# Kernel optimization log

Measured on AMD Instinct MI355X. Metric: run time of the kernel, lower is better.

Reference implementation:

```python
import jax, jax.numpy as jnp
import numpy as np

N, E, H, C, G = 10000, 20000, 12, 768, 64  # nodes, edges, heads, per-head dim, graphs
NEG_SLOPE = 0.2


def _gat_layer(x, W, a_src, a_dst, b, src, dst):
    # x: [N, 768], W: [768, H*C], a_src/a_dst: [H, C], b: [C]
    h = (x @ W).reshape(-1, H, C)                      # [N, H, C]
    s = jnp.einsum('nhc,hc->nh', h, a_src)             # alpha_src per node
    d = jnp.einsum('nhc,hc->nh', h, a_dst)             # alpha_dst per node
    e = jax.nn.leaky_relu(s[src] + d[dst], NEG_SLOPE)  # [Etot, H]
    # segment softmax over incoming edges of each destination node
    m = jax.lax.stop_gradient(jax.ops.segment_max(e, dst, num_segments=N))
    ex = jnp.exp(e - m[dst])
    den = jax.ops.segment_sum(ex, dst, num_segments=N)
    alpha = ex / (den[dst] + 1e-16)                    # [Etot, H]
    out = jax.ops.segment_sum(h[src] * alpha[:, :, None], dst, num_segments=N)
    return out.mean(axis=1) + b                        # concat=False -> head mean, [N, C]


def setup_inputs() -> dict:
    key = jax.random.key(0)
    ks = jax.random.split(key, 16)
    sc = 0.02
    f32 = jnp.float32
    return {
        'x': jax.random.normal(ks[0], (N, 768), f32),
        'edge_index': jax.random.randint(ks[1], (2, E), 0, N),
        'batch': jnp.sort(jax.random.randint(ks[2], (N,), 0, G)),
        'W1': (jax.random.normal(ks[3], (768, H * C), f32) * sc),
        'a_src1': (jax.random.normal(ks[4], (H, C), f32) * sc),
        'a_dst1': (jax.random.normal(ks[5], (H, C), f32) * sc),
        'b1': jnp.zeros((C,), f32),
        'W2': (jax.random.normal(ks[6], (768, H * C), f32) * sc),
        'a_src2': (jax.random.normal(ks[7], (H, C), f32) * sc),
        'a_dst2': (jax.random.normal(ks[8], (H, C), f32) * sc),
        'b2': jnp.zeros((C,), f32),
        'mlp_w1': (jax.random.normal(ks[9], (768, 128), f32) * sc),
        'mlp_b1': jnp.zeros((128,), f32),
        'mlp_w2': (jax.random.normal(ks[10], (128, 4), f32) * sc),
        'mlp_b2': jnp.zeros((4,), f32),
    }


def reference(x, edge_index, batch, W1, a_src1, a_dst1, b1, W2, a_src2, a_dst2, b2,
              mlp_w1, mlp_b1, mlp_w2, mlp_b2):
    loops = jnp.arange(N)                               # GATConv add_self_loops=True
    src = jnp.concatenate([edge_index[0], loops])
    dst = jnp.concatenate([edge_index[1], loops])
    h = _gat_layer(x, W1, a_src1, a_dst1, b1, src, dst)
    h = _gat_layer(h, W2, a_src2, a_dst2, b2, src, dst)
    # scatter_mean over graph assignment
    ssum = jax.ops.segment_sum(h, batch, num_segments=G)
    cnt = jax.ops.segment_sum(jnp.ones((N,), h.dtype), batch, num_segments=G)
    g = ssum / jnp.maximum(cnt, 1.0)[:, None]           # [G, 768]
    z = jax.nn.relu(g @ mlp_w1 + mlp_b1)
    return z @ mlp_w2 + mlp_b2                          # [G, 4] logits
```

## Files before the change

kernel.cpp:

```cpp
#include <hip/hip_runtime.h>
#include <stdint.h>

typedef unsigned short u16;
typedef unsigned int   u32;

#define NNODES 10000
#define NEDGES 20000
#define ETOT   30000
#define NHEADS 12
#define CDIM   768
#define FDIM   768
#define KDIM   9216
#define NGRAPH 64
#define MPAD   10112
#define NEG_SLOPE 0.2f
#define DMAX   32

typedef __attribute__((ext_vector_type(8))) short short8;
typedef __attribute__((ext_vector_type(4))) float f32x4;

__device__ __forceinline__ u16 f32_bf16(float f) {
  u32 u = __float_as_uint(f);
  u = (u + 0x7FFFu + ((u >> 16) & 1u)) >> 16;
  return (u16)u;
}
__device__ __forceinline__ float bf16_f32(u16 v) {
  return __uint_as_float(((u32)v) << 16);
}

__global__ void k_count(const int* __restrict__ dste, int* __restrict__ counts) {
  int e = blockIdx.x * blockDim.x + threadIdx.x;
  if (e >= ETOT) return;
  int dst;
  if (e < NEDGES) dst = dste[e]; else dst = e - NEDGES;
  atomicAdd(&counts[dst], 1);
}

__global__ void k_scan(const int* __restrict__ counts, int* __restrict__ offs) {
  __shared__ int part[256];
  int t = threadIdx.x;
  const int chunk = 40;
  int beg = t * chunk;
  int end = beg + chunk; if (end > NNODES) end = NNODES;
  int s = 0;
  for (int i = beg; i < end && i < NNODES; i++) s += counts[i];
  part[t] = s;
  __syncthreads();
  for (int d = 1; d < 256; d <<= 1) {
    int v = (t >= d) ? part[t - d] : 0;
    __syncthreads();
    part[t] += v;
    __syncthreads();
  }
  int base = (t == 0) ? 0 : part[t - 1];
  for (int i = beg; i < end && i < NNODES; i++) { offs[i] = base; base += counts[i]; }
  if (t == 255) offs[NNODES] = base;
}

__global__ void k_seed(const int* __restrict__ offs, int* __restrict__ cursor) {
  int n = blockIdx.x * blockDim.x + threadIdx.x;
  if (n < NNODES) cursor[n] = offs[n];
}

__global__ void k_scatter(const int* __restrict__ dste, int* __restrict__ cursor,
                          int* __restrict__ elist) {
  int e = blockIdx.x * blockDim.x + threadIdx.x;
  if (e >= ETOT) return;
  int dst;
  if (e < NEDGES) dst = dste[e]; else dst = e - NEDGES;
  int pos = atomicAdd(&cursor[dst], 1);
  elist[pos] = e;
}

__global__ void k_U(const float* __restrict__ W, const float* __restrict__ a_src,
                    const float* __restrict__ a_dst, float* __restrict__ Ut) {
  int k = blockIdx.x;
  int t = threadIdx.x, w = t >> 6, l = t & 63;
  const float* Wrow = W + (size_t)k * KDIM;
#pragma unroll
  for (int q = 0; q < 6; q++) {
    int o = w * 6 + q;
    int h = (o < 12) ? o : o - 12;
    const float* av = (o < 12) ? (a_src + h * CDIM) : (a_dst + h * CDIM);
    const float* wr = Wrow + h * CDIM;
    float p = 0.f;
    for (int c = l; c < CDIM; c += 64) p += wr[c] * av[c];
#pragma unroll
    for (int d = 32; d > 0; d >>= 1) p += __shfl_down(p, d, 64);
    if (l == 0) Ut[o * FDIM + k] = p;
  }
}

__global__ void k_sd(const float* __restrict__ xin, const float* __restrict__ Ut,
                     float* __restrict__ sd, u16* __restrict__ xbf) {
  __shared__ float UtS[24 * FDIM];
  int t = threadIdx.x, w = t >> 6, l = t & 63;
  const float4* U4 = (const float4*)Ut;
  float4* S4 = (float4*)UtS;
  for (int i = t; i < 24 * FDIM / 4; i += 256) S4[i] = U4[i];
  __syncthreads();
#pragma unroll
  for (int rep = 0; rep < 5; rep++) {
    int n = blockIdx.x * 20 + w * 5 + rep;
    if (n >= NNODES) continue;
    const float* xr = xin + (size_t)n * FDIM;
    float4 x0 = *(const float4*)(xr + 4 * l);
    float4 x1 = *(const float4*)(xr + 4 * l + 256);
    float4 x2 = *(const float4*)(xr + 4 * l + 512);
    u16* xb = xbf + (size_t)n * FDIM + 4 * l;
    ushort4 p0, p1, p2;
    p0.x = f32_bf16(x0.x); p0.y = f32_bf16(x0.y); p0.z = f32_bf16(x0.z); p0.w = f32_bf16(x0.w);
    p1.x = f32_bf16(x1.x); p1.y = f32_bf16(x1.y); p1.z = f32_bf16(x1.z); p1.w = f32_bf16(x1.w);
    p2.x = f32_bf16(x2.x); p2.y = f32_bf16(x2.y); p2.z = f32_bf16(x2.z); p2.w = f32_bf16(x2.w);
    *(ushort4*)xb = p0;
    *(ushort4*)(xb + 256) = p1;
    *(ushort4*)(xb + 512) = p2;
#pragma unroll
    for (int o = 0; o < 24; o++) {
      const float4* up = (const float4*)(UtS + o * FDIM + 4 * l);
      float4 u0 = up[0];
      float4 u1 = up[64];
      float4 u2 = up[128];
      float a = x0.x * u0.x + x0.y * u0.y + x0.z * u0.z + x0.w * u0.w
              + x1.x * u1.x + x1.y * u1.y + x1.z * u1.z + x1.w * u1.w
              + x2.x * u2.x + x2.y * u2.y + x2.z * u2.z + x2.w * u2.w;
#pragma unroll
      for (int d = 32; d > 0; d >>= 1) a += __shfl_xor(a, d, 64);
      if (l == 0) sd[n * 24 + o] = a;
    }
  }
}

__global__ void k_trans(const float* __restrict__ W, u16* __restrict__ Bt) {
  int kt = blockIdx.x * 32, jt = blockIdx.y * 32;
  int tx = threadIdx.x, ty = threadIdx.y;
  __shared__ float tile[32][33];
#pragma unroll
  for (int r = 0; r < 4; r++)
    tile[ty + 8 * r][tx] = W[(size_t)(kt + ty + 8 * r) * KDIM + jt + tx];
  __syncthreads();
#pragma unroll
  for (int r = 0; r < 4; r++)
    Bt[(size_t)(jt + ty + 8 * r) * FDIM + kt + tx] = f32_bf16(tile[tx][ty + 8 * r]);
}

__global__ __launch_bounds__(256, 2) void k_gemm(const u16* __restrict__ A,
    const u16* __restrict__ B, u16* __restrict__ C) {
  __shared__ __align__(16) u16 As[2][128 * 32];
  __shared__ __align__(16) u16 Bs[2][256 * 32];
  int t = threadIdx.x;
  int w = t >> 6, l = t & 63;
  int col0 = blockIdx.x * 256;
  int row0 = blockIdx.y * 128;
  int wm = (w >> 1) * 64;
  int wn = (w & 1) * 128;
  f32x4 acc[4][8] = {};
  int idx0 = t * 8;
  int idx1 = idx0 + 2048;
  const u16* Ag0 = A + (size_t)(row0 + (idx0 >> 5)) * FDIM + (idx0 & 31);
  const u16* Ag1 = A + (size_t)(row0 + (idx1 >> 5)) * FDIM + (idx1 & 31);
  const u16* Bg0 = B + (size_t)(col0 + (idx0 >> 5)) * FDIM + (idx0 & 31);
  const u16* Bg1 = B + (size_t)(col0 + ((idx0 + 2048) >> 5)) * FDIM + (idx0 & 31);
  const u16* Bg2 = B + (size_t)(col0 + ((idx0 + 4096) >> 5)) * FDIM + (idx0 & 31);
  const u16* Bg3 = B + (size_t)(col0 + ((idx0 + 6144) >> 5)) * FDIM + (idx0 & 31);
  int lr = l & 15, lk = (l >> 4) * 8;

  short8 ra0, ra1, rb0, rb1, rb2, rb3;
  auto gload = [&](int k0) {
    ra0 = *(const short8*)(Ag0 + k0);
    ra1 = *(const short8*)(Ag1 + k0);
    rb0 = *(const short8*)(Bg0 + k0);
    rb1 = *(const short8*)(Bg1 + k0);
    rb2 = *(const short8*)(Bg2 + k0);
    rb3 = *(const short8*)(Bg3 + k0);
  };
  auto swrite = [&](int buf) {
    *(short8*)(&As[buf][idx0]) = ra0;
    *(short8*)(&As[buf][idx1]) = ra1;
    *(short8*)(&Bs[buf][idx0]) = rb0;
    *(short8*)(&Bs[buf][idx0 + 2048]) = rb1;
    *(short8*)(&Bs[buf][idx0 + 4096]) = rb2;
    *(short8*)(&Bs[buf][idx0 + 6144]) = rb3;
  };

  gload(0);
  swrite(0);
  gload(32);
  __syncthreads();
  const int NIT = FDIM / 32;
  int cur = 0;
  for (int it = 0; it < NIT; it++) {
    short8 af[4], bf[8];
#pragma unroll
    for (int i = 0; i < 4; i++) af[i] = *(const short8*)(&As[cur][(wm + i * 16 + lr) * 32 + lk]);
#pragma unroll
    for (int j = 0; j < 8; j++) bf[j] = *(const short8*)(&Bs[cur][(wn + j * 16 + lr) * 32 + lk]);
#pragma unroll
    for (int i = 0; i < 4; i++)
#pragma unroll
      for (int j = 0; j < 8; j++)
        acc[i][j] = __builtin_amdgcn_mfma_f32_16x16x32_bf16(af[i], bf[j], acc[i][j], 0, 0, 0);
    if (it + 1 < NIT) {
      swrite(cur ^ 1);
      if (it + 2 < NIT) gload((it + 2) * 32);
    }
    __syncthreads();
    cur ^= 1;
  }

  int lg = l >> 4;
#pragma unroll
  for (int i = 0; i < 4; i++)
#pragma unroll
    for (int j = 0; j < 8; j++) {
      int col = col0 + wn + j * 16 + lr;
#pragma unroll
      for (int r = 0; r < 4; r++) {
        int row = row0 + wm + i * 16 + lg * 4 + r;
        C[(size_t)row * KDIM + col] = f32_bf16(acc[i][j][r]);
      }
    }
}

__global__ void k_att(const u16* __restrict__ Hbig, const int* __restrict__ ei,
                      const int* __restrict__ offs, const int* __restrict__ elist,
                      const float* __restrict__ sd, const float* __restrict__ bias,
                      float* __restrict__ out) {
  int t = threadIdx.x, w = t >> 6, l = t & 63;
  int n = blockIdx.x * 4 + w;
  __shared__ int   srcsS[4][DMAX];
  __shared__ float alphS[4][NHEADS * DMAX];
  if (n >= NNODES) return;
  int* srcs = srcsS[w];
  float* alph = alphS[w];
  int beg = offs[n];
  int deg = offs[n + 1] - beg;
  if (deg > DMAX) deg = DMAX;
  if (l < deg) {
    int e = elist[beg + l];
    srcs[l] = (e < NEDGES) ? ei[e] : e - NEDGES;
  }
  __builtin_amdgcn_wave_barrier();
  for (int p = l; p < deg * NHEADS; p += 64) {
    int i = p / NHEADS, h = p - i * NHEADS;
    float v = sd[srcs[i] * 24 + h] + sd[n * 24 + 12 + h];
    v = (v > 0.f) ? v : NEG_SLOPE * v;
    alph[h * DMAX + i] = v;
  }
  __builtin_amdgcn_wave_barrier();
  if (l < NHEADS) {
    float m = -1e30f;
    for (int i = 0; i < deg; i++) m = fmaxf(m, alph[l * DMAX + i]);
    float s = 0.f;
    for (int i = 0; i < deg; i++) {
      float ex = expf(alph[l * DMAX + i] - m);
      alph[l * DMAX + i] = ex;
      s += ex;
    }
    float inv = 1.f / (s + 1e-16f);
    for (int i = 0; i < deg; i++) alph[l * DMAX + i] *= inv;
  }
  __builtin_amdgcn_wave_barrier();
#pragma unroll
  for (int pass = 0; pass < 3; pass++) {
    float4 acc = make_float4(0.f, 0.f, 0.f, 0.f);
    for (int i = 0; i < deg; i++) {
      const u16* hb = Hbig + (size_t)srcs[i] * KDIM + pass * 256 + 4 * l;
#pragma unroll
      for (int h = 0; h < NHEADS; h++) {
        ushort4 hv = *(const ushort4*)(hb + h * CDIM);
        float a = alph[h * DMAX + i];
        acc.x += a * bf16_f32(hv.x);
        acc.y += a * bf16_f32(hv.y);
        acc.z += a * bf16_f32(hv.z);
        acc.w += a * bf16_f32(hv.w);
      }
    }
    int c = pass * 256 + 4 * l;
    const float sc = 1.f / 12.f;
    float4 ov;
    ov.x = acc.x * sc + bias[c + 0];
    ov.y = acc.y * sc + bias[c + 1];
    ov.z = acc.z * sc + bias[c + 2];
    ov.w = acc.w * sc + bias[c + 3];
    *(float4*)(out + (size_t)n * FDIM + c) = ov;
  }
}

__global__ void k_pool(const float* __restrict__ h2, const int* __restrict__ batch,
                       float* __restrict__ g) {
  int gi = blockIdx.x;
  int c = blockIdx.y * 256 + threadIdx.x;
  int lo = 0, hi = NNODES;
  while (lo < hi) { int mid = (lo + hi) >> 1; if (batch[mid] < gi) lo = mid + 1; else hi = mid; }
  int start = lo;
  lo = start; hi = NNODES;
  while (lo < hi) { int mid = (lo + hi) >> 1; if (batch[mid] < gi + 1) lo = mid + 1; else hi = mid; }
  int end = lo;
  int cnt = end - start; if (cnt < 1) cnt = 1;
  float inv = 1.f / (float)cnt;
  float s = 0.f;
  for (int n = start; n < end; n++) s += h2[(size_t)n * FDIM + c];
  g[gi * FDIM + c] = s * inv;
}

__global__ void k_mlp(const float* __restrict__ g, const float* __restrict__ w1,
                      const float* __restrict__ b1, const float* __restrict__ w2,
                      const float* __restrict__ b2, float* __restrict__ out) {
  int gi = blockIdx.x;
  int t = threadIdx.x;
  __shared__ float gs[FDIM];
  __shared__ float zs[128];
  for (int i = t; i < FDIM; i += 128) gs[i] = g[gi * FDIM + i];
  __syncthreads();
  float a = b1[t];
  for (int k = 0; k < FDIM; k++) a += gs[k] * w1[k * 128 + t];
  zs[t] = (a > 0.f) ? a : 0.f;
  __syncthreads();
  if (t < 4) {
    float o = b2[t];
    for (int i = 0; i < 128; i++) o += zs[i] * w2[i * 4 + t];
    out[gi * 4 + t] = o;
  }
}

extern "C" void kernel_launch(void* const* d_in, const int* in_sizes, int n_in,
                              void* d_out, int out_size, void* d_ws, size_t ws_size,
                              hipStream_t stream) {
  const float* x    = (const float*)d_in[0];
  const int*   ei   = (const int*)d_in[1];
  const int*   batch= (const int*)d_in[2];
  const float* W1   = (const float*)d_in[3];
  const float* as1  = (const float*)d_in[4];
  const float* ad1  = (const float*)d_in[5];
  const float* b1   = (const float*)d_in[6];
  const float* W2   = (const float*)d_in[7];
  const float* as2  = (const float*)d_in[8];
  const float* ad2  = (const float*)d_in[9];
  const float* b2   = (const float*)d_in[10];
  const float* mw1  = (const float*)d_in[11];
  const float* mb1  = (const float*)d_in[12];
  const float* mw2  = (const float*)d_in[13];
  const float* mb2  = (const float*)d_in[14];
  float* out = (float*)d_out;
  (void)in_sizes; (void)n_in; (void)out_size; (void)ws_size;

  char* wsb = (char*)d_ws;
  size_t off = 0;
  auto alloc = [&](size_t bytes) -> void* {
    void* p = wsb + off;
    off += (bytes + 255) & ~(size_t)255;
    return p;
  };
  u16*  Hbig   = (u16*)alloc((size_t)MPAD * KDIM * 2);
  u16*  Bt     = (u16*)alloc((size_t)KDIM * FDIM * 2);
  float* h1    = (float*)alloc((size_t)NNODES * FDIM * 4);
  float* h2    = (float*)alloc((size_t)NNODES * FDIM * 4);
  u16*  xbf    = (u16*)h2;
  float* sd    = (float*)alloc((size_t)NNODES * 24 * 4);
  float* Ut    = (float*)alloc((size_t)FDIM * 24 * 4);
  int*  counts = (int*)alloc((size_t)NNODES * 4);
  int*  offs   = (int*)alloc((size_t)(NNODES + 1) * 4);
  int*  cursor = (int*)alloc((size_t)NNODES * 4);
  int*  elist  = (int*)alloc((size_t)ETOT * 4);
  float* gbuf  = (float*)alloc((size_t)NGRAPH * FDIM * 4);

  hipMemsetAsync(counts, 0, NNODES * 4, stream);
  k_count<<<(ETOT + 255) / 256, 256, 0, stream>>>(ei + NEDGES, counts);
  k_scan<<<1, 256, 0, stream>>>(counts, offs);
  k_seed<<<(NNODES + 255) / 256, 256, 0, stream>>>(offs, cursor);
  k_scatter<<<(ETOT + 255) / 256, 256, 0, stream>>>(ei + NEDGES, cursor, elist);

  for (int layer = 0; layer < 2; layer++) {
    const float* xin  = layer ? h1  : x;
    const float* W    = layer ? W2  : W1;
    const float* asrc = layer ? as2 : as1;
    const float* adst = layer ? ad2 : ad1;
    const float* bb   = layer ? b2  : b1;
    float* hout       = layer ? h2  : h1;

    k_U<<<FDIM, 256, 0, stream>>>(W, asrc, adst, Ut);
    k_sd<<<(NNODES + 19) / 20, 256, 0, stream>>>(xin, Ut, sd, xbf);
    k_trans<<<dim3(FDIM / 32, KDIM / 32), dim3(32, 8), 0, stream>>>(W, Bt);
    k_gemm<<<dim3(KDIM / 256, MPAD / 128), 256, 0, stream>>>(xbf, Bt, Hbig);
    k_att<<<(NNODES + 3) / 4, 256, 0, stream>>>(Hbig, ei, offs, elist, sd, bb, hout);
  }

  k_pool<<<dim3(NGRAPH, 3), 256, 0, stream>>>(h2, batch, gbuf);
  k_mlp<<<NGRAPH, 128, 0, stream>>>(gbuf, mw1, mb1, mw2, mb2, out);
}
```

Before: 877.0 us.

## Pre-pack GEMM operands into MFMA fragment layout and drop LDS staging

The producer kernels (k_sd for activations, k_trans for weights) now write bf16 operands directly in a 16-row by 32-k fragment-packed layout. Each lane can then load its MFMA operand with one contiguous 16-byte global load. The GEMM drops its shared-memory double buffer and barriers and reads fragments straight from global memory/L2 on every k-step. This removes LDS traffic and synchronisation, but gives up intra-block reuse through LDS and relies on the cache to serve the repeated fragment loads, with no explicit prefetch.

```diff
diff --git a/kernel.cpp b/kernel.cpp
--- a/kernel.cpp
+++ b/kernel.cpp
@@ -13,6 +13,7 @@
 #define KDIM   9216
 #define NGRAPH 64
 #define MPAD   10112
+#define KT     24
 #define NEG_SLOPE 0.2f
 #define DMAX   32
 
@@ -27,6 +28,7 @@
 __device__ __forceinline__ float bf16_f32(u16 v) {
   return __uint_as_float(((u32)v) << 16);
 }
+
 
 __global__ void k_count(const int* __restrict__ dste, int* __restrict__ counts) {
   int e = blockIdx.x * blockDim.x + threadIdx.x;
@@ -92,7 +94,7 @@
 }
 
 __global__ void k_sd(const float* __restrict__ xin, const float* __restrict__ Ut,
-                     float* __restrict__ sd, u16* __restrict__ xbf) {
+                     float* __restrict__ sd, u16* __restrict__ Ap) {
   __shared__ float UtS[24 * FDIM];
   int t = threadIdx.x, w = t >> 6, l = t & 63;
   const float4* U4 = (const float4*)Ut;
@@ -107,14 +109,18 @@
     float4 x0 = *(const float4*)(xr + 4 * l);
     float4 x1 = *(const float4*)(xr + 4 * l + 256);
     float4 x2 = *(const float4*)(xr + 4 * l + 512);
-    u16* xb = xbf + (size_t)n * FDIM + 4 * l;
-    ushort4 p0, p1, p2;
-    p0.x = f32_bf16(x0.x); p0.y = f32_bf16(x0.y); p0.z = f32_bf16(x0.z); p0.w = f32_bf16(x0.w);
-    p1.x = f32_bf16(x1.x); p1.y = f32_bf16(x1.y); p1.z = f32_bf16(x1.z); p1.w = f32_bf16(x1.w);
-    p2.x = f32_bf16(x2.x); p2.y = f32_bf16(x2.y); p2.z = f32_bf16(x2.z); p2.w = f32_bf16(x2.w);
-    *(ushort4*)xb = p0;
-    *(ushort4*)(xb + 256) = p1;
-    *(ushort4*)(xb + 512) = p2;
+    int fr = n >> 4, rl = n & 15;
+    float4 xv[3] = {x0, x1, x2};
+#pragma unroll
+    for (int c = 0; c < 3; c++) {
+      int k0 = 4 * l + c * 256;
+      ushort4 pk;
+      pk.x = f32_bf16(xv[c].x); pk.y = f32_bf16(xv[c].y);
+      pk.z = f32_bf16(xv[c].z); pk.w = f32_bf16(xv[c].w);
+      u16* dst = Ap + ((size_t)fr * KT + (k0 >> 5)) * 512
+               + ((rl + 16 * ((k0 >> 3) & 3)) << 3) + (k0 & 7);
+      *(ushort4*)dst = pk;
+    }
 #pragma unroll
     for (int o = 0; o < 24; o++) {
       const float4* up = (const float4*)(UtS + o * FDIM + 4 * l);
@@ -131,7 +137,7 @@
   }
 }
 
-__global__ void k_trans(const float* __restrict__ W, u16* __restrict__ Bt) {
+__global__ void k_trans(const float* __restrict__ W, u16* __restrict__ Bp) {
   int kt = blockIdx.x * 32, jt = blockIdx.y * 32;
   int tx = threadIdx.x, ty = threadIdx.y;
   __shared__ float tile[32][33];
@@ -139,76 +145,55 @@
   for (int r = 0; r < 4; r++)
     tile[ty + 8 * r][tx] = W[(size_t)(kt + ty + 8 * r) * KDIM + jt + tx];
   __syncthreads();
-#pragma unroll
-  for (int r = 0; r < 4; r++)
-    Bt[(size_t)(jt + ty + 8 * r) * FDIM + kt + tx] = f32_bf16(tile[tx][ty + 8 * r]);
-}
-
-__global__ __launch_bounds__(256, 2) void k_gemm(const u16* __restrict__ A,
-    const u16* __restrict__ B, u16* __restrict__ C) {
-  __shared__ __align__(16) u16 As[2][128 * 32];
-  __shared__ __align__(16) u16 Bs[2][256 * 32];
+  int j = jt + tx;
+  int k0 = kt + 4 * ty;
+  ushort4 pk;
+  pk.x = f32_bf16(tile[4 * ty + 0][tx]);
+  pk.y = f32_bf16(tile[4 * ty + 1][tx]);
+  pk.z = f32_bf16(tile[4 * ty + 2][tx]);
+  pk.w = f32_bf16(tile[4 * ty + 3][tx]);
+  u16* dst = Bp + ((size_t)(j >> 4) * KT + (k0 >> 5)) * 512
+           + (((j & 15) + 16 * ((k0 >> 3) & 3)) << 3) + (k0 & 7);
+  *(ushort4*)dst = pk;
+}
+
+__global__ __launch_bounds__(256, 2) void k_gemm(const u16* __restrict__ Ap,
+    const u16* __restrict__ Bp, u16* __restrict__ C) {
   int t = threadIdx.x;
   int w = t >> 6, l = t & 63;
   int col0 = blockIdx.x * 256;
   int row0 = blockIdx.y * 128;
   int wm = (w >> 1) * 64;
   int wn = (w & 1) * 128;
+  const short8* Av = (const short8*)Ap + l;
+  const short8* Bv = (const short8*)Bp + l;
+  int fA = ((row0 + wm) >> 4) * KT;
+  int fB = ((col0 + wn) >> 4) * KT;
   f32x4 acc[4][8] = {};
-  int idx0 = t * 8;
-  int idx1 = idx0 + 2048;
-  const u16* Ag0 = A + (size_t)(row0 + (idx0 >> 5)) * FDIM + (idx0 & 31);
-  const u16* Ag1 = A + (size_t)(row0 + (idx1 >> 5)) * FDIM + (idx1 & 31);
-  const u16* Bg0 = B + (size_t)(col0 + (idx0 >> 5)) * FDIM + (idx0 & 31);
-  const u16* Bg1 = B + (size_t)(col0 + ((idx0 + 2048) >> 5)) * FDIM + (idx0 & 31);
-  const u16* Bg2 = B + (size_t)(col0 + ((idx0 + 4096) >> 5)) * FDIM + (idx0 & 31);
-  const u16* Bg3 = B + (size_t)(col0 + ((idx0 + 6144) >> 5)) * FDIM + (idx0 & 31);
-  int lr = l & 15, lk = (l >> 4) * 8;
-
-  short8 ra0, ra1, rb0, rb1, rb2, rb3;
-  auto gload = [&](int k0) {
-    ra0 = *(const short8*)(Ag0 + k0);
-    ra1 = *(const short8*)(Ag1 + k0);
-    rb0 = *(const short8*)(Bg0 + k0);
-    rb1 = *(const short8*)(Bg1 + k0);
-    rb2 = *(const short8*)(Bg2 + k0);
-    rb3 = *(const short8*)(Bg3 + k0);
-  };
-  auto swrite = [&](int buf) {
-    *(short8*)(&As[buf][idx0]) = ra0;
-    *(short8*)(&As[buf][idx1]) = ra1;
-    *(short8*)(&Bs[buf][idx0]) = rb0;
-    *(short8*)(&Bs[buf][idx0 + 2048]) = rb1;
-    *(short8*)(&Bs[buf][idx0 + 4096]) = rb2;
-    *(short8*)(&Bs[buf][idx0 + 6144]) = rb3;
-  };
-
-  gload(0);
-  swrite(0);
-  gload(32);
-  __syncthreads();
-  const int NIT = FDIM / 32;
-  int cur = 0;
-  for (int it = 0; it < NIT; it++) {
-    short8 af[4], bf[8];
-#pragma unroll
-    for (int i = 0; i < 4; i++) af[i] = *(const short8*)(&As[cur][(wm + i * 16 + lr) * 32 + lk]);
-#pragma unroll
-    for (int j = 0; j < 8; j++) bf[j] = *(const short8*)(&Bs[cur][(wn + j * 16 + lr) * 32 + lk]);
+
+  for (int kt = 0; kt < KT; kt++) {
+    short8 a0 = Av[(size_t)(fA + 0 * KT + kt) * 64];
+    short8 a1 = Av[(size_t)(fA + 1 * KT + kt) * 64];
+    short8 a2 = Av[(size_t)(fA + 2 * KT + kt) * 64];
+    short8 a3 = Av[(size_t)(fA + 3 * KT + kt) * 64];
+    short8 b0 = Bv[(size_t)(fB + 0 * KT + kt) * 64];
+    short8 b1 = Bv[(size_t)(fB + 1 * KT + kt) * 64];
+    short8 b2 = Bv[(size_t)(fB + 2 * KT + kt) * 64];
+    short8 b3 = Bv[(size_t)(fB + 3 * KT + kt) * 64];
+    short8 b4 = Bv[(size_t)(fB + 4 * KT + kt) * 64];
+    short8 b5 = Bv[(size_t)(fB + 5 * KT + kt) * 64];
+    short8 b6 = Bv[(size_t)(fB + 6 * KT + kt) * 64];
+    short8 b7 = Bv[(size_t)(fB + 7 * KT + kt) * 64];
+    short8 av[4] = {a0, a1, a2, a3};
+    short8 bv[8] = {b0, b1, b2, b3, b4, b5, b6, b7};
 #pragma unroll
     for (int i = 0; i < 4; i++)
 #pragma unroll
       for (int j = 0; j < 8; j++)
-        acc[i][j] = __builtin_amdgcn_mfma_f32_16x16x32_bf16(af[i], bf[j], acc[i][j], 0, 0, 0);
-    if (it + 1 < NIT) {
-      swrite(cur ^ 1);
-      if (it + 2 < NIT) gload((it + 2) * 32);
-    }
-    __syncthreads();
-    cur ^= 1;
-  }
-
-  int lg = l >> 4;
+        acc[i][j] = __builtin_amdgcn_mfma_f32_16x16x32_bf16(av[i], bv[j], acc[i][j], 0, 0, 0);
+  }
+
+  int lr = l & 15, lg = l >> 4;
 #pragma unroll
   for (int i = 0; i < 4; i++)
 #pragma unroll
@@ -353,10 +338,10 @@
     return p;
   };
   u16*  Hbig   = (u16*)alloc((size_t)MPAD * KDIM * 2);
-  u16*  Bt     = (u16*)alloc((size_t)KDIM * FDIM * 2);
+  u16*  Bp     = (u16*)alloc((size_t)KDIM * FDIM * 2);
   float* h1    = (float*)alloc((size_t)NNODES * FDIM * 4);
   float* h2    = (float*)alloc((size_t)NNODES * FDIM * 4);
-  u16*  xbf    = (u16*)h2;
+  u16*  Ap     = (u16*)h2;
   float* sd    = (float*)alloc((size_t)NNODES * 24 * 4);
   float* Ut    = (float*)alloc((size_t)FDIM * 24 * 4);
   int*  counts = (int*)alloc((size_t)NNODES * 4);
@@ -380,9 +365,9 @@
     float* hout       = layer ? h2  : h1;
 
     k_U<<<FDIM, 256, 0, stream>>>(W, asrc, adst, Ut);
-    k_sd<<<(NNODES + 19) / 20, 256, 0, stream>>>(xin, Ut, sd, xbf);
-    k_trans<<<dim3(FDIM / 32, KDIM / 32), dim3(32, 8), 0, stream>>>(W, Bt);
-    k_gemm<<<dim3(KDIM / 256, MPAD / 128), 256, 0, stream>>>(xbf, Bt, Hbig);
+    k_sd<<<(NNODES + 19) / 20, 256, 0, stream>>>(xin, Ut, sd, Ap);
+    k_trans<<<dim3(FDIM / 32, KDIM / 32), dim3(32, 8), 0, stream>>>(W, Bp);
+    k_gemm<<<dim3(KDIM / 256, MPAD / 128), 256, 0, stream>>>(Ap, Bp, Hbig);
     k_att<<<(NNODES + 3) / 4, 256, 0, stream>>>(Hbig, ei, offs, elist, sd, bb, hout);
   }
 
```

New measurement: 888.3 us. No clear change (+1.3%).
